# Performance work log

Measured on AMD Instinct MI355X. Metric: run time of the kernel, lower is better.

## Reference

```python
import jax, jax.numpy as jnp
import numpy as np


def setup_inputs() -> dict:
    key = jax.random.key(0)
    k1, k2, k3 = jax.random.split(key, 3)
    B, H, W = 4, 1024, 1024
    GD, GH, GW = 8, 16, 16
    NIN, NOUT = 3, 3
    grid = jax.random.normal(k1, (B, (NIN + 1) * NOUT, GD, GH, GW), dtype=jnp.float32)
    guide = jax.random.uniform(k2, (B, 1, H, W), dtype=jnp.float32)  # in [0,1)
    image = jax.random.uniform(k3, (B, NIN, H, W), dtype=jnp.float32)
    return {"grid": grid, "guide": guide, "image": image}


def _bilateral_slice_apply(grid, guide, image):
    """HDRNet bilateral slice + per-pixel affine apply.

    grid:  [B, (n_in+1)*n_out, gd, gh, gw]
    guide: [B, 1, H, W], values in [0, 1]
    image: [B, n_in, H, W]
    out:   [B, n_out, H, W]
    """
    B, C, GD, GH, GW = grid.shape
    _, NIN, H, W = image.shape
    NOUT = C // (NIN + 1)

    # Continuous grid coordinates (HDRNet convention: sample at pixel centers,
    # shifted by -0.5 so tent weights are centered on grid cells).
    gx = (jnp.arange(W, dtype=jnp.float32) + 0.5) * (GW / W) - 0.5  # [W]
    gy = (jnp.arange(H, dtype=jnp.float32) + 0.5) * (GH / H) - 0.5  # [H]
    gz = guide[:, 0] * GD - 0.5                                      # [B,H,W]

    fx, fy, fz = jnp.floor(gx), jnp.floor(gy), jnp.floor(gz)

    def gather_corner(g, zi, yi, xi):
        # g: [C,gd,gh,gw]; zi: [H,W]; yi: [H]; xi: [W] -> [C,H,W]
        return g[:, zi, yi[:, None], xi[None, :]]

    gather_b = jax.vmap(gather_corner, in_axes=(0, 0, None, None))

    acc = jnp.zeros((B, C, H, W), dtype=grid.dtype)
    for dz in (0.0, 1.0):
        zf = fz + dz
        wz = jnp.maximum(1.0 - jnp.abs(zf - gz), 0.0)               # [B,H,W]
        zi = jnp.clip(zf, 0, GD - 1).astype(jnp.int32)
        for dy in (0.0, 1.0):
            yf = fy + dy
            wy = jnp.maximum(1.0 - jnp.abs(yf - gy), 0.0)           # [H]
            yi = jnp.clip(yf, 0, GH - 1).astype(jnp.int32)
            for dx in (0.0, 1.0):
                xf = fx + dx
                wx = jnp.maximum(1.0 - jnp.abs(xf - gx), 0.0)       # [W]
                xi = jnp.clip(xf, 0, GW - 1).astype(jnp.int32)
                w = wz * (wy[:, None] * wx[None, :])                # [B,H,W]
                corner = gather_b(grid, zi, yi, xi)                 # [B,C,H,W]
                acc = acc + w[:, None] * corner

    # Per-pixel affine: out[o] = sum_j A[o,j] * in[j] + A[o,n_in]
    coeffs = acc.reshape(B, NOUT, NIN + 1, H, W)
    out = jnp.einsum('bojhw,bjhw->bohw', coeffs[:, :, :NIN], image) + coeffs[:, :, NIN]
    return out


def reference(grid, guide, image):
    return _bilateral_slice_apply(grid, guide, image)
```

## Files before the change

kernel.cpp:

```cpp
#include <hip/hip_runtime.h>
#include <hip/hip_fp16.h>

#define BATCH 4
#define HH 1024
#define WW 1024
#define GDp 8
#define NC 12
#define CELL2 7
#define HROW2 169

__global__ __launch_bounds__(256, 4) void bsa_kernel(
    const float* __restrict__ grid,
    const float* __restrict__ guide,
    const float* __restrict__ image,
    float* __restrict__ out)
{
    __shared__ float   sg[GDp][3][3][NC];
    __shared__ __half2 Hs2[16][HROW2];

    const int bx = blockIdx.x;
    const int by = blockIdx.y;
    const int b  = blockIdx.z;
    const int tx = threadIdx.x;
    const int ty = threadIdx.y;
    const int tid = ty * 16 + tx;

    const int x0 = bx * 64;
    const int y0 = by * 16;
    const float inv64 = 1.0f / 64.0f;

    const float gy0 = (y0 + 0.5f) * inv64 - 0.5f;
    const int ylo = (int)floorf(gy0);

    const int y = y0 + ty;
    const int xloc = 4 * tx;
    const size_t plane = (size_t)HH * WW;
    const size_t gpix = ((size_t)(b * HH + y)) * WW + x0 + xloc;
    const size_t ib   = (size_t)b * 3 * plane + (size_t)y * WW + x0 + xloc;
    const float4 g4  = *(const float4*)&guide[gpix];
    const float4 im0 = *(const float4*)&image[ib];
    const float4 im1 = *(const float4*)&image[ib + plane];
    const float4 im2 = *(const float4*)&image[ib + 2 * plane];

    {
        const int z = tid >> 5;
        const int u = tid & 31;
        if (u < 27) {
            const int cell = (u * 11) >> 5;
            const int cq   = u - cell * 3;
            const int yy   = (cell * 11) >> 5;
            const int xx   = cell - yy * 3;
            const int gxi = min(max(bx - 1 + xx, 0), 15);
            const int gyi = min(max(ylo + yy, 0), 15);
            const float* gp = grid + (size_t)b * (NC * GDp * 256)
                                   + ((size_t)z * 16 + gyi) * 16 + gxi;
#pragma unroll
            for (int j = 0; j < 4; ++j) {
                const int c = cq * 4 + j;
                const int pos = (c < 8) ? ((c & 3) * 2 + (c >> 2)) : c;
                sg[z][yy][xx][pos] = gp[(size_t)c * (GDp * 256)];
            }
        }
    }
    __syncthreads();

    for (int e = tid; e < 384; e += 256) {
        const int r    = e & 15;
        const int cell = e >> 4;
        const int xs   = cell >> 3;
        const int z    = cell & 7;
        const float gy  = (y0 + r + 0.5f) * inv64 - 0.5f;
        const float fyf = floorf(gy);
        const float wy1 = gy - fyf;
        const float wy0 = 1.0f - wy1;
        const int ys0 = (int)fyf - ylo;
        const float* s0 = &sg[z][ys0][xs][0];
        const float* s1 = &sg[z][ys0 + 1][xs][0];
        __half2* hd = &Hs2[r][cell * CELL2];
#pragma unroll
        for (int m = 0; m < 6; ++m) {
            hd[m] = __floats2half2_rn(wy0 * s0[2*m]   + wy1 * s1[2*m],
                                      wy0 * s0[2*m+1] + wy1 * s1[2*m+1]);
        }
    }
    __syncthreads();

    const int xs0 = tx >> 3;
    const float fxf = (float)(bx - 1 + xs0);
    const float gxb = (x0 + xloc + 0.5f) * inv64 - 0.5f;
    const __half2* Hrow = &Hs2[ty][0];

    const float gk[4]  = {g4.x, g4.y, g4.z, g4.w};
    const float ia[4]  = {im0.x, im0.y, im0.z, im0.w};
    const float ja[4]  = {im1.x, im1.y, im1.z, im1.w};
    const float ka[4]  = {im2.x, im2.y, im2.z, im2.w};
    float ok0[4], ok1[4], ok2[4];

    const __half oneh = __float2half_rn(1.0f);

#pragma unroll
    for (int k = 0; k < 4; ++k) {
        const float wx1 = (gxb - fxf) + (float)k * inv64;
        const float wx0 = 1.0f - wx1;

        const float gz  = fmaf(gk[k], 8.0f, -0.5f);
        const float fzf = floorf(gz);
        const float zpf = fminf(fmaxf(fzf, 0.0f), 6.0f);
        const float whi = fminf(fmaxf(gz - zpf, 0.0f), 1.0f);
        const float wlo = 1.0f - whi;
        const int zp = (int)zpf;

        const __half2 w00 = __float2half2_rn(wx0 * wlo);
        const __half2 w10 = __float2half2_rn(wx0 * whi);
        const __half2 w01 = __float2half2_rn(wx1 * wlo);
        const __half2 w11 = __float2half2_rn(wx1 * whi);

        const __half2* q = Hrow + (xs0 * 8 + zp) * CELL2;
        const __half2 A0 = q[0],  A1 = q[1],  A2 = q[2],  A3 = q[3],  A4 = q[4],  A5 = q[5];
        const __half2 B0 = q[7],  B1 = q[8],  B2 = q[9],  B3 = q[10], B4 = q[11], B5 = q[12];
        const __half2 C0 = q[56], C1 = q[57], C2 = q[58], C3 = q[59], C4 = q[60], C5 = q[61];
        const __half2 D0 = q[63], D1 = q[64], D2 = q[65], D3 = q[66], D4 = q[67], D5 = q[68];

        const __half2 r0 = __hfma2(w00, A0, __hfma2(w10, B0, __hfma2(w01, C0, __hmul2(w11, D0))));
        const __half2 r1 = __hfma2(w00, A1, __hfma2(w10, B1, __hfma2(w01, C1, __hmul2(w11, D1))));
        const __half2 r2 = __hfma2(w00, A2, __hfma2(w10, B2, __hfma2(w01, C2, __hmul2(w11, D2))));
        const __half2 r3 = __hfma2(w00, A3, __hfma2(w10, B3, __hfma2(w01, C3, __hmul2(w11, D3))));
        const __half2 r4 = __hfma2(w00, A4, __hfma2(w10, B4, __hfma2(w01, C4, __hmul2(w11, D4))));
        const __half2 r5 = __hfma2(w00, A5, __hfma2(w10, B5, __hfma2(w01, C5, __hmul2(w11, D5))));

        const __half i0h = __float2half_rn(ia[k]);
        const __half i1h = __float2half_rn(ja[k]);
        const __half i2h = __float2half_rn(ka[k]);
        const __half2 bi0 = __half2half2(i0h);
        const __half2 bi1 = __half2half2(i1h);
        const __half2 bi2 = __half2half2(i2h);

        const __half2 acc01 = __hfma2(bi0, r0, __hfma2(bi1, r1, __hfma2(bi2, r2, r3)));
        const __half2 d2 = __hfma2(__halves2half2(i0h, i1h), r4,
                                   __hmul2(__halves2half2(i2h, oneh), r5));

        ok0[k] = __low2float(acc01);
        ok1[k] = __high2float(acc01);
        ok2[k] = __half2float(__hadd(__low2half(d2), __high2half(d2)));
    }

    *(float4*)&out[ib]             = make_float4(ok0[0], ok0[1], ok0[2], ok0[3]);
    *(float4*)&out[ib + plane]     = make_float4(ok1[0], ok1[1], ok1[2], ok1[3]);
    *(float4*)&out[ib + 2 * plane] = make_float4(ok2[0], ok2[1], ok2[2], ok2[3]);
}

extern "C" void kernel_launch(void* const* d_in, const int* in_sizes, int n_in,
                              void* d_out, int out_size, void* d_ws, size_t ws_size,
                              hipStream_t stream) {
    const float* grid  = (const float*)d_in[0];
    const float* guide = (const float*)d_in[1];
    const float* image = (const float*)d_in[2];
    float* out = (float*)d_out;

    dim3 block(16, 16, 1);
    dim3 grid_dim(WW / 64, HH / 16, BATCH);
    bsa_kernel<<<grid_dim, block, 0, stream>>>(grid, guide, image, out);
}
```

Baseline: 26.09 us.

## Double tile height to 32 rows and use nontemporal loads/stores

Each block now covers 32 rows instead of 16, using 512 threads, which amortizes the grid staging and the y-interpolated half table over more pixels. Global loads of guide and image and stores of the output use nontemporal builtins to avoid polluting the cache with streaming data. The image-to-half conversions are also packed slightly differently. Larger blocks raise per-block shared memory and may reduce the number of blocks, which could lower occupancy and tail balance.

```diff
diff --git a/kernel.cpp b/kernel.cpp
--- a/kernel.cpp
+++ b/kernel.cpp
@@ -8,15 +8,18 @@
 #define NC 12
 #define CELL2 7
 #define HROW2 169
+#define TILEY 32
 
-__global__ __launch_bounds__(256, 4) void bsa_kernel(
+typedef float f4 __attribute__((ext_vector_type(4)));
+
+__global__ __launch_bounds__(512, 4) void bsa_kernel(
     const float* __restrict__ grid,
     const float* __restrict__ guide,
     const float* __restrict__ image,
     float* __restrict__ out)
 {
     __shared__ float   sg[GDp][3][3][NC];
-    __shared__ __half2 Hs2[16][HROW2];
+    __shared__ __half2 Hs2[TILEY][HROW2];
 
     const int bx = blockIdx.x;
     const int by = blockIdx.y;
@@ -26,7 +29,7 @@
     const int tid = ty * 16 + tx;
 
     const int x0 = bx * 64;
-    const int y0 = by * 16;
+    const int y0 = by * TILEY;
     const float inv64 = 1.0f / 64.0f;
 
     const float gy0 = (y0 + 0.5f) * inv64 - 0.5f;
@@ -37,12 +40,12 @@
     const size_t plane = (size_t)HH * WW;
     const size_t gpix = ((size_t)(b * HH + y)) * WW + x0 + xloc;
     const size_t ib   = (size_t)b * 3 * plane + (size_t)y * WW + x0 + xloc;
-    const float4 g4  = *(const float4*)&guide[gpix];
-    const float4 im0 = *(const float4*)&image[ib];
-    const float4 im1 = *(const float4*)&image[ib + plane];
-    const float4 im2 = *(const float4*)&image[ib + 2 * plane];
+    const f4 g4  = __builtin_nontemporal_load((const f4*)&guide[gpix]);
+    const f4 im0 = __builtin_nontemporal_load((const f4*)&image[ib]);
+    const f4 im1 = __builtin_nontemporal_load((const f4*)&image[ib + plane]);
+    const f4 im2 = __builtin_nontemporal_load((const f4*)&image[ib + 2 * plane]);
 
-    {
+    if (tid < 256) {
         const int z = tid >> 5;
         const int u = tid & 31;
         if (u < 27) {
@@ -64,9 +67,9 @@
     }
     __syncthreads();
 
-    for (int e = tid; e < 384; e += 256) {
-        const int r    = e & 15;
-        const int cell = e >> 4;
+    for (int e = tid; e < 24 * TILEY; e += 512) {
+        const int r    = e & (TILEY - 1);
+        const int cell = e >> 5;
         const int xs   = cell >> 3;
         const int z    = cell & 7;
         const float gy  = (y0 + r + 0.5f) * inv64 - 0.5f;
@@ -95,8 +98,6 @@
     const float ja[4]  = {im1.x, im1.y, im1.z, im1.w};
     const float ka[4]  = {im2.x, im2.y, im2.z, im2.w};
     float ok0[4], ok1[4], ok2[4];
-
-    const __half oneh = __float2half_rn(1.0f);
 
 #pragma unroll
     for (int k = 0; k < 4; ++k) {
@@ -128,25 +129,26 @@
         const __half2 r4 = __hfma2(w00, A4, __hfma2(w10, B4, __hfma2(w01, C4, __hmul2(w11, D4))));
         const __half2 r5 = __hfma2(w00, A5, __hfma2(w10, B5, __hfma2(w01, C5, __hmul2(w11, D5))));
 
-        const __half i0h = __float2half_rn(ia[k]);
-        const __half i1h = __float2half_rn(ja[k]);
-        const __half i2h = __float2half_rn(ka[k]);
-        const __half2 bi0 = __half2half2(i0h);
-        const __half2 bi1 = __half2half2(i1h);
-        const __half2 bi2 = __half2half2(i2h);
+        const __half2 bi0 = __float2half2_rn(ia[k]);
+        const __half2 bi1 = __float2half2_rn(ja[k]);
+        const __half2 bi2 = __float2half2_rn(ka[k]);
+        const __half2 p01 = __floats2half2_rn(ia[k], ja[k]);
+        const __half2 p21 = __floats2half2_rn(ka[k], 1.0f);
 
         const __half2 acc01 = __hfma2(bi0, r0, __hfma2(bi1, r1, __hfma2(bi2, r2, r3)));
-        const __half2 d2 = __hfma2(__halves2half2(i0h, i1h), r4,
-                                   __hmul2(__halves2half2(i2h, oneh), r5));
+        const __half2 d2 = __hfma2(p01, r4, __hmul2(p21, r5));
 
         ok0[k] = __low2float(acc01);
         ok1[k] = __high2float(acc01);
         ok2[k] = __half2float(__hadd(__low2half(d2), __high2half(d2)));
     }
 
-    *(float4*)&out[ib]             = make_float4(ok0[0], ok0[1], ok0[2], ok0[3]);
-    *(float4*)&out[ib + plane]     = make_float4(ok1[0], ok1[1], ok1[2], ok1[3]);
-    *(float4*)&out[ib + 2 * plane] = make_float4(ok2[0], ok2[1], ok2[2], ok2[3]);
+    const f4 o0 = {ok0[0], ok0[1], ok0[2], ok0[3]};
+    const f4 o1 = {ok1[0], ok1[1], ok1[2], ok1[3]};
+    const f4 o2 = {ok2[0], ok2[1], ok2[2], ok2[3]};
+    __builtin_nontemporal_store(o0, (f4*)&out[ib]);
+    __builtin_nontemporal_store(o1, (f4*)&out[ib + plane]);
+    __builtin_nontemporal_store(o2, (f4*)&out[ib + 2 * plane]);
 }
 
 extern "C" void kernel_launch(void* const* d_in, const int* in_sizes, int n_in,
@@ -157,7 +159,7 @@
     const float* image = (const float*)d_in[2];
     float* out = (float*)d_out;
 
-    dim3 block(16, 16, 1);
-    dim3 grid_dim(WW / 64, HH / 16, BATCH);
+    dim3 block(16, 32, 1);
+    dim3 grid_dim(WW / 64, HH / TILEY, BATCH);
     bsa_kernel<<<grid_dim, block, 0, stream>>>(grid, guide, image, out);
 }
```

After: 27.11 us. 3.9% more time.
